# Performance work log

Hardware: AMD Instinct MI355X
Metric: run time of the kernel (lower is better)

Reference implementation:

```python
import jax, jax.numpy as jnp
import numpy as np

EMBED, HEADS, LEVELS, POINTS = 256, 8, 4, 4
SPATIAL_SHAPES = np.array([[128, 128], [64, 64], [32, 32], [16, 16]], dtype=np.int32)


def _grid_init_bias():
    # Faithful reproduction of the sampling_offsets bias init (per-head directional grid).
    thetas = np.arange(HEADS, dtype=np.float32) * (2.0 * np.pi / HEADS)
    g = np.stack([np.cos(thetas), np.sin(thetas)], -1)
    g = g / np.abs(g).max(-1, keepdims=True)
    g = np.tile(g.reshape(HEADS, 1, 1, 2), (1, LEVELS, POINTS, 1))
    for i in range(POINTS):
        g[:, :, i, :] *= i + 1
    return g.reshape(-1).astype(np.float32)


def setup_inputs() -> dict:
    key = jax.random.key(0)
    ks = jax.random.split(key, 8)
    bs = 2
    V = int((SPATIAL_SHAPES[:, 0] * SPATIAL_SHAPES[:, 1]).sum())  # 21760
    Q = V  # encoder self-attention
    C = EMBED
    n_off = HEADS * LEVELS * POINTS * 2
    n_attn = HEADS * LEVELS * POINTS
    inv_sqrt_c = 1.0 / np.sqrt(C)
    return {
        "query": jax.random.normal(ks[0], (bs, Q, C), jnp.float32),
        "value": jax.random.normal(ks[1], (bs, V, C), jnp.float32),
        "reference_points": jax.random.uniform(ks[2], (bs, Q, LEVELS, 2), jnp.float32),
        "spatial_shapes": SPATIAL_SHAPES,  # static int array
        # learned parameters (torch Linear stored as [in, out]: y = x @ W + b)
        "W_off": jax.random.normal(ks[3], (C, n_off), jnp.float32) * 0.01,
        "b_off": jnp.asarray(_grid_init_bias()),
        "W_attn": jax.random.normal(ks[4], (C, n_attn), jnp.float32) * 0.02,
        "b_attn": jnp.zeros((n_attn,), jnp.float32),
        "W_v": jax.random.normal(ks[5], (C, C), jnp.float32) * inv_sqrt_c,
        "b_v": jnp.zeros((C,), jnp.float32),
        "W_out": jax.random.normal(ks[6], (C, C), jnp.float32) * inv_sqrt_c,
        "b_out": jnp.zeros((C,), jnp.float32),
    }


def _ms_deform_attn(query, value, reference_points, shapes,
                    W_off, b_off, W_attn, b_attn, W_v, b_v, W_out, b_out):
    bs, Q, C = query.shape
    d = C // HEADS
    # value projection -> [bs, heads, V, d]
    val = (value @ W_v + b_v).reshape(bs, -1, HEADS, d).transpose(0, 2, 1, 3)
    # sampling offsets and attention weights from query
    off = (query @ W_off + b_off).reshape(bs, Q, HEADS, LEVELS, POINTS, 2)
    attn = jax.nn.softmax(
        (query @ W_attn + b_attn).reshape(bs, Q, HEADS, LEVELS * POINTS), axis=-1
    ).reshape(bs, Q, HEADS, LEVELS, POINTS)
    # offset normalizer is (W, H) per level
    norm = jnp.asarray(np.stack([shapes[:, 1], shapes[:, 0]], -1), jnp.float32)  # [L,2]
    loc = reference_points[:, :, None, :, None, :] + off / norm[None, None, None, :, None, :]

    out = jnp.zeros((bs, HEADS, Q, d), query.dtype)
    start = 0
    for l in range(LEVELS):
        H, W = int(shapes[l, 0]), int(shapes[l, 1])
        v_l = val[:, :, start:start + H * W]  # [bs, heads, H*W, d]
        start += H * W
        loc_l = loc[:, :, :, l]    # [bs, Q, heads, P, 2] in [0,1]
        attn_l = attn[:, :, :, l]  # [bs, Q, heads, P]
        # grid_sample(align_corners=False, padding_mode='zeros') semantics
        g = 2.0 * loc_l - 1.0
        x = (g[..., 0] + 1.0) * 0.5 * W - 0.5
        y = (g[..., 1] + 1.0) * 0.5 * H - 0.5
        x0 = jnp.floor(x)
        y0 = jnp.floor(y)
        for dx in (0, 1):
            for dy in (0, 1):
                xi = x0 + dx
                yi = y0 + dy
                w = (1.0 - jnp.abs(x - xi)) * (1.0 - jnp.abs(y - yi))
                valid = (xi >= 0) & (xi <= W - 1) & (yi >= 0) & (yi <= H - 1)
                w = jnp.where(valid, w, 0.0) * attn_l  # fused corner + attention weight
                idx = (jnp.clip(yi, 0, H - 1).astype(jnp.int32) * W
                       + jnp.clip(xi, 0, W - 1).astype(jnp.int32))  # [bs,Q,heads,P]
                idx_t = jnp.transpose(idx, (0, 2, 1, 3)).reshape(bs, HEADS, Q * POINTS)
                vals = jnp.take_along_axis(v_l, idx_t[..., None], axis=2)
                vals = vals.reshape(bs, HEADS, Q, POINTS, d)
                out = out + jnp.einsum('bhqpd,bqhp->bhqd', vals, w)
    out = out.transpose(0, 2, 1, 3).reshape(bs, Q, C)  # heads-major channel layout
    return out @ W_out + b_out


def reference(query, value, reference_points, spatial_shapes,
              W_off, b_off, W_attn, b_attn, W_v, b_v, W_out, b_out):
    shapes = np.asarray(spatial_shapes)  # static
    return _ms_deform_attn(query, value, reference_points, shapes,
                           W_off, b_off, W_attn, b_attn, W_v, b_v, W_out, b_out)
```

## Files before the change

kernel.cpp:

```cpp
#include <hip/hip_runtime.h>
#include <hip/hip_cooperative_groups.h>
#include <math.h>

namespace cg = cooperative_groups;

#define QN 21760
#define MTOT 43520
#define SZBQC 11141120

typedef __attribute__((ext_vector_type(8))) short bf16x8;
typedef __attribute__((ext_vector_type(4))) float f32x4;

__device__ inline ushort f2bf(float f) {
  union { float f; uint u; } v; v.f = f;
  return (ushort)((v.u + 0x7FFFu + ((v.u >> 16) & 1u)) >> 16);
}
__device__ inline uint pk2(float lo, float hi) { return (uint)f2bf(lo) | ((uint)f2bf(hi) << 16); }

__device__ inline void g2l(const ushort* g, ushort* l) {
  __builtin_amdgcn_global_load_lds(
      (const __attribute__((address_space(1))) void*)g,
      (__attribute__((address_space(3))) void*)l, 16, 0, 0);
}


__device__ __forceinline__ void prep_body(
    int bidx, int t,
    const float* __restrict__ Wv, const float* __restrict__ Wout,
    const float* __restrict__ Woff, const float* __restrict__ Wattn,
    const float* __restrict__ boff, const float* __restrict__ battn,
    ushort* __restrict__ wv_t, ushort* __restrict__ wout_t,
    ushort* __restrict__ wol_t, float* __restrict__ biasf) {
  if (bidx < 256) {
    int idx = bidx * 256 + t; int n = idx >> 8, k = idx & 255;
    wv_t[idx] = f2bf(Wv[(size_t)k * 256 + n]);
  } else if (bidx < 512) {
    int idx = (bidx - 256) * 256 + t; int n = idx >> 8, k = idx & 255;
    wout_t[idx] = f2bf(Wout[(size_t)k * 256 + n]);
  } else {
    int idx = (bidx - 512) * 256 + t; int n = idx >> 8, k = idx & 255;
    float v = (n < 256) ? Woff[(size_t)k * 256 + n] : Wattn[(size_t)k * 128 + (n - 256)];
    wol_t[idx] = f2bf(v);
    if (idx < 384) biasf[idx] = (idx < 256) ? boff[idx] : battn[idx - 256];
  }
}


__device__ __forceinline__ void gemm_in_body(
    ushort (*As)[4096], ushort (*Bs)[4096], int bxv, int bx, int t,
    const float* __restrict__ value, const float* __restrict__ query,
    const ushort* __restrict__ Wv, const ushort* __restrict__ Wol,
    const float* __restrict__ bv, const float* __restrict__ bol,
    ushort* __restrict__ val_out, float* __restrict__ offlog) {
  const int wave = t >> 6, lane = t & 63;
  const int bm = bxv * 128;
  const bool isVal = bx < 2;
  const float* A   = isVal ? value : query;
  const ushort* Bt = isVal ? (Wv + (size_t)bx * 128 * 256)
                           : (Wol + (size_t)(bx - 2) * 128 * 256);
  const int wm = (wave >> 1) * 64, wn = (wave & 1) * 64;
  const int l15 = lane & 15, l4 = lane >> 4;
  const int pc = l4 ^ ((l15 >> 1) & 3);

  const int srow = lane >> 2;
  const int sch  = (lane & 3) ^ ((lane >> 3) & 3);
  const ushort* Bg = Bt + (size_t)(32 * wave + srow) * 256 + sch * 8;
  ushort* lb[2] = { &Bs[0][(32 * wave) * 32], &Bs[1][(32 * wave) * 32] };

  f32x4 acc[4][4];
#pragma unroll
  for (int i = 0; i < 4; ++i)
#pragma unroll
    for (int j = 0; j < 4; ++j) acc[i][j] = (f32x4){0.f, 0.f, 0.f, 0.f};

  int arow[4], apart[4];
#pragma unroll
  for (int i = 0; i < 4; ++i) {
    int c = t + i * 256; arow[i] = c >> 3; apart[i] = c & 7;
  }

  {
    float4 pa[4];
#pragma unroll
    for (int i = 0; i < 4; ++i)
      pa[i] = *(const float4*)&A[(size_t)(bm + arow[i]) * 256 + apart[i] * 4];
    g2l(Bg, lb[0]); g2l(Bg + 16 * 256, lb[0] + 16 * 32);
#pragma unroll
    for (int i = 0; i < 4; ++i) {
      int pc16 = (apart[i] >> 1) ^ ((arow[i] >> 1) & 3);
      ushort4 hv = { f2bf(pa[i].x), f2bf(pa[i].y), f2bf(pa[i].z), f2bf(pa[i].w) };
      *(ushort4*)&As[0][arow[i] * 32 + pc16 * 8 + (apart[i] & 1) * 4] = hv;
    }
  }

  for (int k = 0; k < 8; ++k) {
    __syncthreads();
    const int cur = k & 1, nxt = cur ^ 1;
    float4 pa[4];
    if (k < 7) {
      int k1 = (k + 1) * 32;
#pragma unroll
      for (int i = 0; i < 4; ++i)
        pa[i] = *(const float4*)&A[(size_t)(bm + arow[i]) * 256 + k1 + apart[i] * 4];
      g2l(Bg + k1, lb[nxt]); g2l(Bg + 16 * 256 + k1, lb[nxt] + 16 * 32);
    }
    bf16x8 af[4], bfr[4];
#pragma unroll
    for (int mi = 0; mi < 4; ++mi)
      af[mi] = *(const bf16x8*)&As[cur][(wm + mi * 16 + l15) * 32 + pc * 8];
#pragma unroll
    for (int ni = 0; ni < 4; ++ni)
      bfr[ni] = *(const bf16x8*)&Bs[cur][(wn + ni * 16 + l15) * 32 + pc * 8];
#pragma unroll
    for (int mi = 0; mi < 4; ++mi)
#pragma unroll
      for (int ni = 0; ni < 4; ++ni)
        acc[mi][ni] = __builtin_amdgcn_mfma_f32_16x16x32_bf16(af[mi], bfr[ni], acc[mi][ni], 0, 0, 0);
    if (k < 7) {
#pragma unroll
      for (int i = 0; i < 4; ++i) {
        int pc16 = (apart[i] >> 1) ^ ((arow[i] >> 1) & 3);
        ushort4 hv = { f2bf(pa[i].x), f2bf(pa[i].y), f2bf(pa[i].z), f2bf(pa[i].w) };
        *(ushort4*)&As[nxt][arow[i] * 32 + pc16 * 8 + (apart[i] & 1) * 4] = hv;
      }
    }
  }

  if (isVal) {
    _Float16* vo = (_Float16*)val_out;
#pragma unroll
    for (int mi = 0; mi < 4; ++mi)
#pragma unroll
      for (int ni = 0; ni < 4; ++ni) {
        int col = bx * 128 + wn + ni * 16 + l15;
        float bb = bv[col];
        int hh = col >> 5, c = col & 31;
#pragma unroll
        for (int r = 0; r < 4; ++r) {
          int row = bm + wm + mi * 16 + l4 * 4 + r;
          int b = (row >= QN) ? 1 : 0;
          int vpos = row - b * QN;
          vo[((size_t)(b * 8 + hh) * QN + vpos) * 32 + c] = (_Float16)(acc[mi][ni][r] + bb);
        }
      }
  } else {
#pragma unroll
    for (int mi = 0; mi < 4; ++mi)
#pragma unroll
      for (int ni = 0; ni < 4; ++ni) {
        int col = (bx - 2) * 128 + wn + ni * 16 + l15;
        float bb = bol[col];
#pragma unroll
        for (int r = 0; r < 4; ++r) {
          int row = bm + wm + mi * 16 + l4 * 4 + r;
          offlog[(size_t)row * 384 + col] = acc[mi][ni][r] + bb;
        }
      }
  }
}

__device__ __forceinline__ void gemm_out_body(
    ushort (*As)[4096], ushort (*Bs)[4096], int bxv, int byv, int t,
    const ushort* __restrict__ A, const ushort* __restrict__ Bt,
    const float* __restrict__ bias, float* __restrict__ C) {
  const int wave = t >> 6, lane = t & 63;
  const int bm = bxv * 128, bn = byv * 128;
  const int wm = (wave >> 1) * 64, wn = (wave & 1) * 64;
  const int l15 = lane & 15, l4 = lane >> 4;
  const int pc = l4 ^ ((l15 >> 1) & 3);

  const int srow = lane >> 2;
  const int sch  = (lane & 3) ^ ((lane >> 3) & 3);
  const ushort* Ag = A + (size_t)(bm + 32 * wave + srow) * 256 + sch * 8;
  const ushort* Bg = Bt + (size_t)(bn + 32 * wave + srow) * 256 + sch * 8;
  ushort* la[2] = { &As[0][(32 * wave) * 32], &As[1][(32 * wave) * 32] };
  ushort* lb[2] = { &Bs[0][(32 * wave) * 32], &Bs[1][(32 * wave) * 32] };

  f32x4 acc[4][4];
#pragma unroll
  for (int i = 0; i < 4; ++i)
#pragma unroll
    for (int j = 0; j < 4; ++j) acc[i][j] = (f32x4){0.f, 0.f, 0.f, 0.f};

  g2l(Ag, la[0]); g2l(Ag + 16 * 256, la[0] + 16 * 32);
  g2l(Bg, lb[0]); g2l(Bg + 16 * 256, lb[0] + 16 * 32);

  for (int k = 0; k < 8; ++k) {
    __syncthreads();
    const int cur = k & 1, nxt = cur ^ 1;
    if (k < 7) {
      int k1 = (k + 1) * 32;
      g2l(Ag + k1, la[nxt]); g2l(Ag + 16 * 256 + k1, la[nxt] + 16 * 32);
      g2l(Bg + k1, lb[nxt]); g2l(Bg + 16 * 256 + k1, lb[nxt] + 16 * 32);
    }
    bf16x8 af[4], bfr[4];
#pragma unroll
    for (int mi = 0; mi < 4; ++mi)
      af[mi] = *(const bf16x8*)&As[cur][(wm + mi * 16 + l15) * 32 + pc * 8];
#pragma unroll
    for (int ni = 0; ni < 4; ++ni)
      bfr[ni] = *(const bf16x8*)&Bs[cur][(wn + ni * 16 + l15) * 32 + pc * 8];
#pragma unroll
    for (int mi = 0; mi < 4; ++mi)
#pragma unroll
      for (int ni = 0; ni < 4; ++ni)
        acc[mi][ni] = __builtin_amdgcn_mfma_f32_16x16x32_bf16(af[mi], bfr[ni], acc[mi][ni], 0, 0, 0);
  }

#pragma unroll
  for (int mi = 0; mi < 4; ++mi)
#pragma unroll
    for (int ni = 0; ni < 4; ++ni) {
      int col = bn + wn + ni * 16 + l15;
      float bb = bias[col];
#pragma unroll
      for (int r = 0; r < 4; ++r) {
        int row = bm + wm + mi * 16 + l4 * 4 + r;
        C[(size_t)row * 256 + col] = acc[mi][ni][r] + bb;
      }
    }
}

__device__ __forceinline__ void fmah(float* a, uint4 u, float wv) {
  union { uint4 u; _Float16 h[8]; } c; c.u = u;
#pragma unroll
  for (int i = 0; i < 8; ++i) a[i] = fmaf((float)c.h[i], wv, a[i]);
}

__device__ __forceinline__ void msda_body(
    int vb, int tix,
    const ushort* __restrict__ val, const float* __restrict__ offlog,
    const float* __restrict__ ref, ushort* __restrict__ interm) {
  int h   = vb & 7;
  int z   = vb >> 3;
  int s   = tix & 7;
  int o   = s & 3;
  int pp  = s >> 2;
  bool xs = s >= 4;
  int bq  = z * 32 + (tix >> 3);
  int b   = (bq >= QN) ? 1 : 0;
  const ushort* vbl = val + (size_t)((uint)(b * 8 + h) * (uint)QN) * 32u + (uint)(s * 8);

  const float* lgp = offlog + (size_t)bq * 384 + 256 + h * 16;
  float2 lg = *(const float2*)(lgp + o * 4 + pp * 2);
  float m = fmaxf(lg.x, lg.y);
  m = fmaxf(m, __shfl_xor(m, 1, 64));
  m = fmaxf(m, __shfl_xor(m, 2, 64));
  m = fmaxf(m, __shfl_xor(m, 4, 64));
  float e0 = __expf(lg.x - m), e1 = __expf(lg.y - m);
  float ssum = e0 + e1;
  ssum += __shfl_xor(ssum, 1, 64);
  ssum += __shfl_xor(ssum, 2, 64);
  ssum += __shfl_xor(ssum, 4, 64);
  float inv = __builtin_amdgcn_rcpf(ssum);
  float aw0 = e0 * inv, aw1 = e1 * inv;

  const int  Wl  = 128 >> o;
  const uint t16 = 65536u >> (o + o);
  const int  lst = (int)((65536u - t16) / 3u);
  const float fW = (float)Wl;
  const float* offp = offlog + (size_t)bq * 384 + h * 32;
  float4 f0 = *(const float4*)(offp + o * 8 + pp * 4);
  float2 rf = *(const float2*)(ref + (size_t)bq * 8 + o * 2);
  const float xb = rf.x * fW - 0.5f;
  const float yb = rf.y * fW - 0.5f;
  float ox[2] = { f0.x, f0.z };
  float oy[2] = { f0.y, f0.w };
  float awq[2] = { aw0, aw1 };

  uint  pA0[2], pA1[2];
  float pW0[2], pW1[2], pY0[2], pY1[2];
#pragma unroll
  for (int q = 0; q < 2; ++q) {
    float x = xb + ox[q], y = yb + oy[q];
    float x0f = floorf(x), y0f = floorf(y);
    float fx = x - x0f, fy = y - y0f;
    int x0 = (int)x0f, y0 = (int)y0f;
    float a = awq[q];
    float wx0 = ((uint)x0       < (uint)Wl) ? (1.f - fx) : 0.f;
    float wx1 = ((uint)(x0 + 1) < (uint)Wl) ? fx         : 0.f;
    pY0[q] = (((uint)y0       < (uint)Wl) ? (1.f - fy) : 0.f) * a;
    pY1[q] = (((uint)(y0 + 1) < (uint)Wl) ? fy         : 0.f) * a;
    int xc0 = min(max(x0, 0), Wl - 1);
    int xc1 = min(max(x0 + 1, 0), Wl - 1);
    int yc0 = min(max(y0, 0), Wl - 1);
    int yc1 = min(max(y0 + 1, 0), Wl - 1);
    int xbase = min(max(x0, 0), Wl - 2);
    pW0[q] = ((xbase     == xc0) ? wx0 : 0.f) + ((xbase     == xc1) ? wx1 : 0.f);
    pW1[q] = ((xbase + 1 == xc0) ? wx0 : 0.f) + ((xbase + 1 == xc1) ? wx1 : 0.f);
    pA0[q] = (uint)((lst + yc0 * Wl + xbase) * 32);
    pA1[q] = (uint)((lst + yc1 * Wl + xbase) * 32);
  }

  float acc[8];
#pragma unroll
  for (int i = 0; i < 8; ++i) acc[i] = 0.f;

  const int gb = (tix & 63) & ~7;

  uint  bA0[2], bA1[2];
  float bW[2], bY0[2], bY1[2];
  uint4 u0[2], u1[2];

#define MSDA_BCAST(J, S) do {                                   \
    const int l_ = (J) >> 2, p_ = (J) & 3;                      \
    const int src_ = gb | ((p_ >> 1) << 2) | l_;                \
    const int q_ = p_ & 1;                                      \
    bA0[S] = (uint)__shfl((int)pA0[q_], src_, 64);              \
    bA1[S] = (uint)__shfl((int)pA1[q_], src_, 64);              \
    float w0_ = __shfl(pW0[q_], src_, 64);                      \
    float w1_ = __shfl(pW1[q_], src_, 64);                      \
    bW[S]  = xs ? w1_ : w0_;                                    \
    bY0[S] = __shfl(pY0[q_], src_, 64);                         \
    bY1[S] = __shfl(pY1[q_], src_, 64);                         \
  } while (0)
#define MSDA_LOAD(S) do {                                       \
    u0[S] = *(const uint4*)(vbl + bA0[S]);                      \
    u1[S] = *(const uint4*)(vbl + bA1[S]);                      \
  } while (0)

  MSDA_BCAST(0, 0);
  MSDA_LOAD(0);
#pragma unroll
  for (int j = 0; j < 16; ++j) {
    const int cur = j & 1, nxt = cur ^ 1;
    if (j < 15) { MSDA_BCAST(j + 1, nxt); MSDA_LOAD(nxt); }
    fmah(acc, u0[cur], bW[cur] * bY0[cur]);
    fmah(acc, u1[cur], bW[cur] * bY1[cur]);
  }
#undef MSDA_BCAST
#undef MSDA_LOAD

#pragma unroll
  for (int i = 0; i < 8; ++i) acc[i] += __shfl_xor(acc[i], 4, 64);

  uint2 ov;
  if (!xs) { ov.x = pk2(acc[0], acc[1]); ov.y = pk2(acc[2], acc[3]); }
  else     { ov.x = pk2(acc[4], acc[5]); ov.y = pk2(acc[6], acc[7]); }
  *(uint2*)(interm + (size_t)bq * 256 + h * 32 + (s & 3) * 8 + (xs ? 4 : 0)) = ov;
}


__global__ __launch_bounds__(256) void prep_weights(
    const float* Wv, const float* Wout, const float* Woff, const float* Wattn,
    const float* boff, const float* battn,
    ushort* wv_t, ushort* wout_t, ushort* wol_t, float* biasf) {
  prep_body(blockIdx.x, threadIdx.x, Wv, Wout, Woff, Wattn, boff, battn,
            wv_t, wout_t, wol_t, biasf);
}

__global__ __launch_bounds__(256) void gemm_in(
    const float* value, const float* query, const ushort* Wv, const ushort* Wol,
    const float* bv, const float* bol, ushort* val_out, float* offlog) {
  __shared__ ushort As[2][4096];
  __shared__ ushort Bs[2][4096];
  gemm_in_body(As, Bs, blockIdx.x, blockIdx.y, threadIdx.x,
               value, query, Wv, Wol, bv, bol, val_out, offlog);
}

__global__ __launch_bounds__(256) void gemm_out(
    const ushort* A, const ushort* Bt, const float* bias, float* C) {
  __shared__ ushort As[2][4096];
  __shared__ ushort Bs[2][4096];
  gemm_out_body(As, Bs, blockIdx.x, blockIdx.y, threadIdx.x, A, Bt, bias, C);
}

__global__ __launch_bounds__(256) void msda_sample(
    const ushort* val, const float* offlog, const float* ref, ushort* interm) {
  msda_body(blockIdx.x, threadIdx.x, val, offlog, ref, interm);
}


struct FusedArgs {
  const float *query, *value, *ref;
  const float *Woff, *boff, *Wattn, *battn, *Wv, *bv, *Wout, *bout;
  ushort *ws_wv, *ws_wol, *ws_wout;
  float *ws_biasf;
  ushort *ws_val, *ws_interm;
  float *ws_offlog;
  float *out;
};

__global__ __launch_bounds__(256) void fused_all(FusedArgs a) {
  __shared__ ushort As[2][4096];
  __shared__ ushort Bs[2][4096];
  cg::grid_group grid = cg::this_grid();
  const int t = threadIdx.x;
  const int g0 = blockIdx.x, gs = gridDim.x;

  for (int vb = g0; vb < 896; vb += gs)
    prep_body(vb, t, a.Wv, a.Wout, a.Woff, a.Wattn, a.boff, a.battn,
              a.ws_wv, a.ws_wout, a.ws_wol, a.ws_biasf);
  __builtin_amdgcn_fence(__ATOMIC_RELEASE, "agent");
  grid.sync();
  __builtin_amdgcn_fence(__ATOMIC_ACQUIRE, "agent");

  for (int vb = g0; vb < 1700; vb += gs) {
    gemm_in_body(As, Bs, vb % 340, vb / 340, t,
                 a.value, a.query, a.ws_wv, a.ws_wol, a.bv, a.ws_biasf,
                 a.ws_val, a.ws_offlog);
    __syncthreads();
  }
  __builtin_amdgcn_fence(__ATOMIC_RELEASE, "agent");
  grid.sync();
  __builtin_amdgcn_fence(__ATOMIC_ACQUIRE, "agent");

  for (int vb = g0; vb < 10880; vb += gs)
    msda_body(vb, t, a.ws_val, a.ws_offlog, a.ref, a.ws_interm);
  __builtin_amdgcn_fence(__ATOMIC_RELEASE, "agent");
  grid.sync();
  __builtin_amdgcn_fence(__ATOMIC_ACQUIRE, "agent");

  for (int vb = g0; vb < 680; vb += gs) {
    gemm_out_body(As, Bs, vb % 340, vb / 340, t,
                  a.ws_interm, a.ws_wout, a.bout, a.out);
    __syncthreads();
  }
}


extern "C" void kernel_launch(void* const* d_in, const int* in_sizes, int n_in,
                              void* d_out, int out_size, void* d_ws, size_t ws_size,
                              hipStream_t stream) {
  const float* query = (const float*)d_in[0];
  const float* value = (const float*)d_in[1];
  const float* ref   = (const float*)d_in[2];
  const float* W_off  = (const float*)d_in[4];
  const float* b_off  = (const float*)d_in[5];
  const float* W_attn = (const float*)d_in[6];
  const float* b_attn = (const float*)d_in[7];
  const float* W_v    = (const float*)d_in[8];
  const float* b_v    = (const float*)d_in[9];
  const float* W_out  = (const float*)d_in[10];
  const float* b_out  = (const float*)d_in[11];
  float* out = (float*)d_out;

  char* wsb = (char*)d_ws;
  ushort* ws_wv     = (ushort*)(wsb + 0);
  ushort* ws_wol    = (ushort*)(wsb + 131072);
  ushort* ws_wout   = (ushort*)(wsb + 327680);
  float*  ws_biasf  = (float*)(wsb + 458752);
  ushort* ws_val    = (ushort*)(wsb + 462848);
  ushort* ws_interm = (ushort*)(wsb + 22745088);
  float*  ws_offlog = (float*)(wsb + 45027328);
  size_t need = (size_t)45027328 + 66846720;
  if (ws_size < need) return;

  dim3 blk(256);

  bool coop_done = false;
  int nb = 0;
  if (hipOccupancyMaxActiveBlocksPerMultiprocessor(&nb, (const void*)fused_all, 256, 0)
          == hipSuccess && nb > 0) {
    int grid = nb * 256;
    if (grid > 4096) grid = 4096;
    FusedArgs fa;
    fa.query = query; fa.value = value; fa.ref = ref;
    fa.Woff = W_off; fa.boff = b_off; fa.Wattn = W_attn; fa.battn = b_attn;
    fa.Wv = W_v; fa.bv = b_v; fa.Wout = W_out; fa.bout = b_out;
    fa.ws_wv = ws_wv; fa.ws_wol = ws_wol; fa.ws_wout = ws_wout;
    fa.ws_biasf = ws_biasf; fa.ws_val = ws_val; fa.ws_interm = ws_interm;
    fa.ws_offlog = ws_offlog; fa.out = out;
    void* kargs[] = { (void*)&fa };
    if (hipLaunchCooperativeKernel((const void*)fused_all, dim3(grid), blk,
                                   kargs, 0, stream) == hipSuccess)
      coop_done = true;
  }

  if (!coop_done) {
    prep_weights<<<dim3(896), blk, 0, stream>>>(W_v, W_out, W_off, W_attn, b_off, b_attn,
                                                ws_wv, ws_wout, ws_wol, ws_biasf);
    gemm_in<<<dim3(340, 5), blk, 0, stream>>>(value, query, ws_wv, ws_wol, b_v, ws_biasf,
                                              ws_val, ws_offlog);
    msda_sample<<<dim3(10880), blk, 0, stream>>>(ws_val, ws_offlog, ref, ws_interm);
    gemm_out<<<dim3(340, 2), blk, 0, stream>>>(ws_interm, ws_wout, b_out, out);
  }
}
```

Measured before the change: 262.2 us.

## Reuse converted A panel across weight panels in input GEMM; triple-buffer output GEMM

The input projection GEMM now stages the whole bf16-converted 128x256 activation panel in LDS once per row block and loops over all weight panels (2 for value, 3 for query). Previously each of five column blocks reloaded and reconverted the same fp32 rows. The output GEMM switches to a three-stage global-to-LDS pipeline with explicit vmcnt waits and one barrier per k-step. The shared allocation grows to 80KB, which can reduce occupancy, and in the cooperative kernel it can shrink the grid for every phase, including sampling.

```diff
diff --git a/kernel.cpp b/kernel.cpp
--- a/kernel.cpp
+++ b/kernel.cpp
@@ -47,31 +47,23 @@
 
 
 __device__ __forceinline__ void gemm_in_body(
-    ushort (*As)[4096], ushort (*Bs)[4096], int bxv, int bx, int t,
+    ushort (*AsF)[4096], ushort (*Bs)[4096], int bxv, int grp, int t,
     const float* __restrict__ value, const float* __restrict__ query,
     const ushort* __restrict__ Wv, const ushort* __restrict__ Wol,
     const float* __restrict__ bv, const float* __restrict__ bol,
     ushort* __restrict__ val_out, float* __restrict__ offlog) {
   const int wave = t >> 6, lane = t & 63;
   const int bm = bxv * 128;
-  const bool isVal = bx < 2;
-  const float* A   = isVal ? value : query;
-  const ushort* Bt = isVal ? (Wv + (size_t)bx * 128 * 256)
-                           : (Wol + (size_t)(bx - 2) * 128 * 256);
+  const float* A = grp ? query : value;
+  const int npan = grp ? 3 : 2;
   const int wm = (wave >> 1) * 64, wn = (wave & 1) * 64;
   const int l15 = lane & 15, l4 = lane >> 4;
   const int pc = l4 ^ ((l15 >> 1) & 3);
 
   const int srow = lane >> 2;
   const int sch  = (lane & 3) ^ ((lane >> 3) & 3);
-  const ushort* Bg = Bt + (size_t)(32 * wave + srow) * 256 + sch * 8;
+  const ushort* Bgbase = (grp ? Wol : Wv) + (size_t)(32 * wave + srow) * 256 + sch * 8;
   ushort* lb[2] = { &Bs[0][(32 * wave) * 32], &Bs[1][(32 * wave) * 32] };
-
-  f32x4 acc[4][4];
-#pragma unroll
-  for (int i = 0; i < 4; ++i)
-#pragma unroll
-    for (int j = 0; j < 4; ++j) acc[i][j] = (f32x4){0.f, 0.f, 0.f, 0.f};
 
   int arow[4], apart[4];
 #pragma unroll
@@ -79,83 +71,88 @@
     int c = t + i * 256; arow[i] = c >> 3; apart[i] = c & 7;
   }
 
-  {
+  g2l(Bgbase, lb[0]); g2l(Bgbase + 16 * 256, lb[0] + 16 * 32);
+
+#pragma unroll
+  for (int k = 0; k < 8; ++k) {
     float4 pa[4];
 #pragma unroll
     for (int i = 0; i < 4; ++i)
-      pa[i] = *(const float4*)&A[(size_t)(bm + arow[i]) * 256 + apart[i] * 4];
-    g2l(Bg, lb[0]); g2l(Bg + 16 * 256, lb[0] + 16 * 32);
+      pa[i] = *(const float4*)&A[(size_t)(bm + arow[i]) * 256 + k * 32 + apart[i] * 4];
 #pragma unroll
     for (int i = 0; i < 4; ++i) {
       int pc16 = (apart[i] >> 1) ^ ((arow[i] >> 1) & 3);
       ushort4 hv = { f2bf(pa[i].x), f2bf(pa[i].y), f2bf(pa[i].z), f2bf(pa[i].w) };
-      *(ushort4*)&As[0][arow[i] * 32 + pc16 * 8 + (apart[i] & 1) * 4] = hv;
-    }
-  }
-
-  for (int k = 0; k < 8; ++k) {
-    __syncthreads();
-    const int cur = k & 1, nxt = cur ^ 1;
-    float4 pa[4];
-    if (k < 7) {
-      int k1 = (k + 1) * 32;
-#pragma unroll
-      for (int i = 0; i < 4; ++i)
-        pa[i] = *(const float4*)&A[(size_t)(bm + arow[i]) * 256 + k1 + apart[i] * 4];
-      g2l(Bg + k1, lb[nxt]); g2l(Bg + 16 * 256 + k1, lb[nxt] + 16 * 32);
-    }
-    bf16x8 af[4], bfr[4];
-#pragma unroll
-    for (int mi = 0; mi < 4; ++mi)
-      af[mi] = *(const bf16x8*)&As[cur][(wm + mi * 16 + l15) * 32 + pc * 8];
-#pragma unroll
-    for (int ni = 0; ni < 4; ++ni)
-      bfr[ni] = *(const bf16x8*)&Bs[cur][(wn + ni * 16 + l15) * 32 + pc * 8];
-#pragma unroll
-    for (int mi = 0; mi < 4; ++mi)
+      *(ushort4*)&AsF[k][arow[i] * 32 + pc16 * 8 + (apart[i] & 1) * 4] = hv;
+    }
+  }
+
+  for (int p = 0; p < npan; ++p) {
+    const ushort* Bg = Bgbase + (size_t)p * 32768;
+    if (p > 0) {
+      g2l(Bg, lb[0]); g2l(Bg + 16 * 256, lb[0] + 16 * 32);
+    }
+
+    f32x4 acc[4][4];
+#pragma unroll
+    for (int i = 0; i < 4; ++i)
+#pragma unroll
+      for (int j = 0; j < 4; ++j) acc[i][j] = (f32x4){0.f, 0.f, 0.f, 0.f};
+
+#pragma unroll
+    for (int k = 0; k < 8; ++k) {
+      __syncthreads();
+      const int cur = k & 1, nxt = cur ^ 1;
+      if (k < 7) {
+        int k1 = (k + 1) * 32;
+        g2l(Bg + k1, lb[nxt]); g2l(Bg + 16 * 256 + k1, lb[nxt] + 16 * 32);
+      }
+      bf16x8 af[4], bfr[4];
+#pragma unroll
+      for (int mi = 0; mi < 4; ++mi)
+        af[mi] = *(const bf16x8*)&AsF[k][(wm + mi * 16 + l15) * 32 + pc * 8];
 #pragma unroll
       for (int ni = 0; ni < 4; ++ni)
-        acc[mi][ni] = __builtin_amdgcn_mfma_f32_16x16x32_bf16(af[mi], bfr[ni], acc[mi][ni], 0, 0, 0);
-    if (k < 7) {
-#pragma unroll
-      for (int i = 0; i < 4; ++i) {
-        int pc16 = (apart[i] >> 1) ^ ((arow[i] >> 1) & 3);
-        ushort4 hv = { f2bf(pa[i].x), f2bf(pa[i].y), f2bf(pa[i].z), f2bf(pa[i].w) };
-        *(ushort4*)&As[nxt][arow[i] * 32 + pc16 * 8 + (apart[i] & 1) * 4] = hv;
-      }
-    }
-  }
-
-  if (isVal) {
-    _Float16* vo = (_Float16*)val_out;
-#pragma unroll
-    for (int mi = 0; mi < 4; ++mi)
-#pragma unroll
-      for (int ni = 0; ni < 4; ++ni) {
-        int col = bx * 128 + wn + ni * 16 + l15;
-        float bb = bv[col];
-        int hh = col >> 5, c = col & 31;
-#pragma unroll
-        for (int r = 0; r < 4; ++r) {
-          int row = bm + wm + mi * 16 + l4 * 4 + r;
-          int b = (row >= QN) ? 1 : 0;
-          int vpos = row - b * QN;
-          vo[((size_t)(b * 8 + hh) * QN + vpos) * 32 + c] = (_Float16)(acc[mi][ni][r] + bb);
+        bfr[ni] = *(const bf16x8*)&Bs[cur][(wn + ni * 16 + l15) * 32 + pc * 8];
+#pragma unroll
+      for (int mi = 0; mi < 4; ++mi)
+#pragma unroll
+        for (int ni = 0; ni < 4; ++ni)
+          acc[mi][ni] = __builtin_amdgcn_mfma_f32_16x16x32_bf16(af[mi], bfr[ni], acc[mi][ni], 0, 0, 0);
+    }
+
+    const int bx = grp ? (2 + p) : p;
+    if (bx < 2) {
+      _Float16* vo = (_Float16*)val_out;
+#pragma unroll
+      for (int mi = 0; mi < 4; ++mi)
+#pragma unroll
+        for (int ni = 0; ni < 4; ++ni) {
+          int col = bx * 128 + wn + ni * 16 + l15;
+          float bb = bv[col];
+          int hh = col >> 5, c = col & 31;
+#pragma unroll
+          for (int r = 0; r < 4; ++r) {
+            int row = bm + wm + mi * 16 + l4 * 4 + r;
+            int b = (row >= QN) ? 1 : 0;
+            int vpos = row - b * QN;
+            vo[((size_t)(b * 8 + hh) * QN + vpos) * 32 + c] = (_Float16)(acc[mi][ni][r] + bb);
+          }
         }
-      }
-  } else {
-#pragma unroll
-    for (int mi = 0; mi < 4; ++mi)
-#pragma unroll
-      for (int ni = 0; ni < 4; ++ni) {
-        int col = (bx - 2) * 128 + wn + ni * 16 + l15;
-        float bb = bol[col];
-#pragma unroll
-        for (int r = 0; r < 4; ++r) {
-          int row = bm + wm + mi * 16 + l4 * 4 + r;
-          offlog[(size_t)row * 384 + col] = acc[mi][ni][r] + bb;
+    } else {
+#pragma unroll
+      for (int mi = 0; mi < 4; ++mi)
+#pragma unroll
+        for (int ni = 0; ni < 4; ++ni) {
+          int col = (bx - 2) * 128 + wn + ni * 16 + l15;
+          float bb = bol[col];
+#pragma unroll
+          for (int r = 0; r < 4; ++r) {
+            int row = bm + wm + mi * 16 + l4 * 4 + r;
+            offlog[(size_t)row * 384 + col] = acc[mi][ni][r] + bb;
+          }
         }
-      }
+    }
   }
 }
 
@@ -173,8 +170,10 @@
   const int sch  = (lane & 3) ^ ((lane >> 3) & 3);
   const ushort* Ag = A + (size_t)(bm + 32 * wave + srow) * 256 + sch * 8;
   const ushort* Bg = Bt + (size_t)(bn + 32 * wave + srow) * 256 + sch * 8;
-  ushort* la[2] = { &As[0][(32 * wave) * 32], &As[1][(32 * wave) * 32] };
-  ushort* lb[2] = { &Bs[0][(32 * wave) * 32], &Bs[1][(32 * wave) * 32] };
+  ushort* la[3] = { &As[0][(32 * wave) * 32], &As[1][(32 * wave) * 32],
+                    &As[2][(32 * wave) * 32] };
+  ushort* lb[3] = { &Bs[0][(32 * wave) * 32], &Bs[1][(32 * wave) * 32],
+                    &Bs[2][(32 * wave) * 32] };
 
   f32x4 acc[4][4];
 #pragma unroll
@@ -182,24 +181,32 @@
 #pragma unroll
     for (int j = 0; j < 4; ++j) acc[i][j] = (f32x4){0.f, 0.f, 0.f, 0.f};
 
-  g2l(Ag, la[0]); g2l(Ag + 16 * 256, la[0] + 16 * 32);
-  g2l(Bg, lb[0]); g2l(Bg + 16 * 256, lb[0] + 16 * 32);
-
+  g2l(Ag, la[0]);      g2l(Ag + 16 * 256, la[0] + 16 * 32);
+  g2l(Bg, lb[0]);      g2l(Bg + 16 * 256, lb[0] + 16 * 32);
+  g2l(Ag + 32, la[1]); g2l(Ag + 16 * 256 + 32, la[1] + 16 * 32);
+  g2l(Bg + 32, lb[1]); g2l(Bg + 16 * 256 + 32, lb[1] + 16 * 32);
+
+#pragma unroll
   for (int k = 0; k < 8; ++k) {
-    __syncthreads();
-    const int cur = k & 1, nxt = cur ^ 1;
-    if (k < 7) {
-      int k1 = (k + 1) * 32;
-      g2l(Ag + k1, la[nxt]); g2l(Ag + 16 * 256 + k1, la[nxt] + 16 * 32);
-      g2l(Bg + k1, lb[nxt]); g2l(Bg + 16 * 256 + k1, lb[nxt] + 16 * 32);
+    const int cb = k % 3;
+    const int sb = (k + 2) % 3;
+    if (k < 7) { asm volatile("s_waitcnt vmcnt(4)" ::: "memory"); }
+    else       { asm volatile("s_waitcnt vmcnt(0)" ::: "memory"); }
+    __builtin_amdgcn_sched_barrier(0);
+    __builtin_amdgcn_s_barrier();
+    __builtin_amdgcn_sched_barrier(0);
+    if (k + 2 <= 7) {
+      int k2 = (k + 2) * 32;
+      g2l(Ag + k2, la[sb]); g2l(Ag + 16 * 256 + k2, la[sb] + 16 * 32);
+      g2l(Bg + k2, lb[sb]); g2l(Bg + 16 * 256 + k2, lb[sb] + 16 * 32);
     }
     bf16x8 af[4], bfr[4];
 #pragma unroll
     for (int mi = 0; mi < 4; ++mi)
-      af[mi] = *(const bf16x8*)&As[cur][(wm + mi * 16 + l15) * 32 + pc * 8];
+      af[mi] = *(const bf16x8*)&As[cb][(wm + mi * 16 + l15) * 32 + pc * 8];
 #pragma unroll
     for (int ni = 0; ni < 4; ++ni)
-      bfr[ni] = *(const bf16x8*)&Bs[cur][(wn + ni * 16 + l15) * 32 + pc * 8];
+      bfr[ni] = *(const bf16x8*)&Bs[cb][(wn + ni * 16 + l15) * 32 + pc * 8];
 #pragma unroll
     for (int mi = 0; mi < 4; ++mi)
 #pragma unroll
@@ -352,16 +359,16 @@
 __global__ __launch_bounds__(256) void gemm_in(
     const float* value, const float* query, const ushort* Wv, const ushort* Wol,
     const float* bv, const float* bol, ushort* val_out, float* offlog) {
-  __shared__ ushort As[2][4096];
+  __shared__ ushort AsF[8][4096];
   __shared__ ushort Bs[2][4096];
-  gemm_in_body(As, Bs, blockIdx.x, blockIdx.y, threadIdx.x,
+  gemm_in_body(AsF, Bs, blockIdx.x, blockIdx.y, threadIdx.x,
                value, query, Wv, Wol, bv, bol, val_out, offlog);
 }
 
 __global__ __launch_bounds__(256) void gemm_out(
     const ushort* A, const ushort* Bt, const float* bias, float* C) {
-  __shared__ ushort As[2][4096];
-  __shared__ ushort Bs[2][4096];
+  __shared__ ushort As[3][4096];
+  __shared__ ushort Bs[3][4096];
   gemm_out_body(As, Bs, blockIdx.x, blockIdx.y, threadIdx.x, A, Bt, bias, C);
 }
 
@@ -382,8 +389,7 @@
 };
 
 __global__ __launch_bounds__(256) void fused_all(FusedArgs a) {
-  __shared__ ushort As[2][4096];
-  __shared__ ushort Bs[2][4096];
+  __shared__ ushort smem[40960];
   cg::grid_group grid = cg::this_grid();
   const int t = threadIdx.x;
   const int g0 = blockIdx.x, gs = gridDim.x;
@@ -395,11 +401,15 @@
   grid.sync();
   __builtin_amdgcn_fence(__ATOMIC_ACQUIRE, "agent");
 
-  for (int vb = g0; vb < 1700; vb += gs) {
-    gemm_in_body(As, Bs, vb % 340, vb / 340, t,
-                 a.value, a.query, a.ws_wv, a.ws_wol, a.bv, a.ws_biasf,
-                 a.ws_val, a.ws_offlog);
-    __syncthreads();
+  {
+    ushort (*AsF)[4096] = (ushort(*)[4096])smem;
+    ushort (*BsI)[4096] = (ushort(*)[4096])(smem + 32768);
+    for (int vb = g0; vb < 680; vb += gs) {
+      gemm_in_body(AsF, BsI, vb % 340, vb / 340, t,
+                   a.value, a.query, a.ws_wv, a.ws_wol, a.bv, a.ws_biasf,
+                   a.ws_val, a.ws_offlog);
+      __syncthreads();
+    }
   }
   __builtin_amdgcn_fence(__ATOMIC_RELEASE, "agent");
   grid.sync();
@@ -411,10 +421,14 @@
   grid.sync();
   __builtin_amdgcn_fence(__ATOMIC_ACQUIRE, "agent");
 
-  for (int vb = g0; vb < 680; vb += gs) {
-    gemm_out_body(As, Bs, vb % 340, vb / 340, t,
-                  a.ws_interm, a.ws_wout, a.bout, a.out);
-    __syncthreads();
+  {
+    ushort (*AsO)[4096] = (ushort(*)[4096])smem;
+    ushort (*BsO)[4096] = (ushort(*)[4096])(smem + 12288);
+    for (int vb = g0; vb < 680; vb += gs) {
+      gemm_out_body(AsO, BsO, vb % 340, vb / 340, t,
+                    a.ws_interm, a.ws_wout, a.bout, a.out);
+      __syncthreads();
+    }
   }
 }
 
@@ -470,7 +484,7 @@
   if (!coop_done) {
     prep_weights<<<dim3(896), blk, 0, stream>>>(W_v, W_out, W_off, W_attn, b_off, b_attn,
                                                 ws_wv, ws_wout, ws_wol, ws_biasf);
-    gemm_in<<<dim3(340, 5), blk, 0, stream>>>(value, query, ws_wv, ws_wol, b_v, ws_biasf,
+    gemm_in<<<dim3(340, 2), blk, 0, stream>>>(value, query, ws_wv, ws_wol, b_v, ws_biasf,
                                               ws_val, ws_offlog);
     msda_sample<<<dim3(10880), blk, 0, stream>>>(ws_val, ws_offlog, ref, ws_interm);
     gemm_out<<<dim3(340, 2), blk, 0, stream>>>(ws_interm, ws_wout, b_out, out);
```

After: 274.9 us. +4.9%, slower.
